# Kernel tuning notes

Hardware: AMD Instinct MI355X
Metric: run time of the kernel (lower is better)

Reference implementation:

```python
import jax, jax.numpy as jnp
import numpy as np

N_NODES = 50000
N_EDGES = 800000
NFEAT, NHID, NCLASS = 512, 128, 40
BN_EPS = 1e-5


def setup_inputs() -> dict:
    key = jax.random.key(0)
    ks = jax.random.split(key, 12)
    x = jax.random.normal(ks[0], (N_NODES, NFEAT), dtype=jnp.float32)
    edge_index = jax.random.randint(ks[1], (2, N_EDGES), 0, N_NODES, dtype=jnp.int64)
    edge_weight = jax.random.uniform(ks[2], (N_EDGES,), dtype=jnp.float32)
    def glorot(k, fi, fo):
        lim = (6.0 / (fi + fo)) ** 0.5
        return jax.random.uniform(k, (fi, fo), minval=-lim, maxval=lim, dtype=jnp.float32)
    return {
        "x": x, "edge_index": edge_index, "edge_weight": edge_weight,
        "W1": glorot(ks[3], NFEAT, NHID), "b1": jnp.zeros((NHID,), jnp.float32),
        "W2": glorot(ks[4], NHID, NHID), "b2": jnp.zeros((NHID,), jnp.float32),
        "W3": glorot(ks[5], NHID, NHID), "b3": jnp.zeros((NHID,), jnp.float32),
        "g1": jnp.ones((NHID,), jnp.float32), "be1": jnp.zeros((NHID,), jnp.float32),
        "g2": jnp.ones((NHID,), jnp.float32), "be2": jnp.zeros((NHID,), jnp.float32),
        "g3": jnp.ones((NHID,), jnp.float32), "be3": jnp.zeros((NHID,), jnp.float32),
        "linW": glorot(ks[6], NHID, NCLASS), "linb": jnp.zeros((NCLASS,), jnp.float32),
    }


def _gcn_norm(edge_index, edge_weight, n):
    # PyG gcn_norm: add self-loops (weight 1), symmetric D^-1/2 (A+I) D^-1/2
    loop = jnp.arange(n, dtype=edge_index.dtype)
    row = jnp.concatenate([edge_index[0], loop])
    col = jnp.concatenate([edge_index[1], loop])
    ew = jnp.concatenate([edge_weight, jnp.ones((n,), edge_weight.dtype)])
    deg = jax.ops.segment_sum(ew, col, num_segments=n)
    dinv = jnp.where(deg > 0, jax.lax.rsqrt(jnp.maximum(deg, 1e-30)), 0.0)
    norm = dinv[row] * ew * dinv[col]
    return row, col, norm


def _conv(x, W, b, row, col, norm, n):
    h = x @ W                                   # [N, out]
    msg = h[row] * norm[:, None]                # gather + weight, [E+N, out]
    return jax.ops.segment_sum(msg, col, num_segments=n) + b


def _bn(x, g, b):
    # training-mode BatchNorm over node dim (biased variance)
    mu = jnp.mean(x, axis=0)
    var = jnp.mean((x - mu) ** 2, axis=0)
    return (x - mu) * jax.lax.rsqrt(var + BN_EPS) * g + b


def reference(x, edge_index, edge_weight, W1, b1, W2, b2, W3, b3,
              g1, be1, g2, be2, g3, be3, linW, linb):
    n = x.shape[0]
    row, col, norm = _gcn_norm(edge_index, edge_weight, n)
    x1 = _bn(jax.nn.relu(_conv(x, W1, b1, row, col, norm, n)), g1, be1)
    x2 = _bn(jax.nn.relu(_conv(x1, W2, b2, row, col, norm, n)), g2, be2)
    x3 = _bn(_conv(x2, W3, b3, row, col, norm, n), g3, be3)
    logits = x3 @ linW + linb
    return (logits, jax.nn.softmax(logits, axis=1), x3)
```

## Files before the change

### kernel.cpp

```cpp
#include <hip/hip_runtime.h>
#include <hip/hip_bf16.h>

#define N_NODES 50000
#define N_EDGES 800000
#define NFEAT 512
#define NHID 128
#define NCLASS 40
#define BN_EPS 1e-5f

typedef __attribute__((ext_vector_type(8))) short short8;
typedef __attribute__((ext_vector_type(4))) float f32x4;

#define GEMM1_BLOCKS ((N_NODES + 127) / 128)
#define GEMMH_BLOCKS ((N_NODES + 127) / 128)
#define EDGE_BLOCKS ((N_EDGES + 255) / 256)
#define SCAN_BLOCKS ((N_NODES + 255) / 256)
#define BN_BLOCKS ((N_NODES + 255) / 256)
#define AGG_BLOCKS ((N_NODES * 64 + 255) / 256)

__device__ __forceinline__ unsigned short f2b(float f) {
    unsigned int u = __float_as_uint(f);
    u += 0x7fff + ((u >> 16) & 1);
    return (unsigned short)(u >> 16);
}
__device__ __forceinline__ unsigned int pk2(float lo, float hi) {
    unsigned int r;
    asm("v_cvt_pk_bf16_f32 %0, %1, %2" : "=v"(r) : "v"(lo), "v"(hi));
    return r;
}
__device__ __forceinline__ float blo(unsigned int v) {
    return __uint_as_float(v << 16);
}
__device__ __forceinline__ float bhi(unsigned int v) {
    return __uint_as_float(v & 0xffff0000u);
}

__global__ void k_prep_w(const float* __restrict__ W1, const float* __restrict__ W2,
                         const float* __restrict__ W3, unsigned short* __restrict__ W1t,
                         unsigned short* __restrict__ W2t, unsigned short* __restrict__ W3t,
                         unsigned long long* __restrict__ degcnt,
                         float* __restrict__ stats, int* __restrict__ syncp) {
    int i = blockIdx.x * blockDim.x + threadIdx.x;
    if (i < N_NODES) degcnt[i] = 0ULL;
    if (i < 768) stats[i] = 0.f;
    else if (i < 776) syncp[i - 768] = 0;
    if (i < 65536) {
        int k = i >> 7, n = i & 127;
        W1t[n * 512 + k] = f2b(W1[i]);
    } else if (i < 81920) {
        int j = i - 65536; int k = j >> 7, n = j & 127;
        W2t[n * 128 + k] = f2b(W2[j]);
    } else if (i < 98304) {
        int j = i - 81920; int k = j >> 7, n = j & 127;
        W3t[n * 128 + k] = f2b(W3[j]);
    }
}

__global__ __launch_bounds__(256) void k_fat(
    const float* __restrict__ x, const unsigned short* __restrict__ W1t,
    unsigned short* __restrict__ hbuf,
    const unsigned int* __restrict__ words, const float* __restrict__ ew,
    int* __restrict__ row, int* __restrict__ col,
    unsigned long long* __restrict__ degcnt, int* __restrict__ slot) {
    __shared__ unsigned short As[128][40];
    __shared__ unsigned short Bs[128][40];
    __shared__ int s_any;
    int tid = threadIdx.x;
    if (blockIdx.x < GEMM1_BLOCKS) {
        int m0 = blockIdx.x * 128;
        int srow = tid >> 1;
        int skh = (tid & 1) << 4;
        int wave = tid >> 6, lane = tid & 63;
        int wm = (wave >> 1) * 64, wn = (wave & 1) * 64;
        int l15 = lane & 15, quad = lane >> 4;
        f32x4 acc[4][4] = {};
        bool arow_ok = (m0 + srow) < N_NODES;
        const float* arow_p = x + (size_t)(m0 + srow) * 512 + skh;
        const unsigned short* wrow_p = W1t + (size_t)srow * 512 + skh;
        float4 ta[4];
        uint4 tb0, tb1;
#pragma unroll
        for (int q = 0; q < 4; q++) {
            ta[q] = make_float4(0.f, 0.f, 0.f, 0.f);
            if (arow_ok) ta[q] = *(const float4*)(arow_p + q * 4);
        }
        tb0 = *(const uint4*)(wrow_p);
        tb1 = *(const uint4*)(wrow_p + 8);
        for (int kt = 0; kt < 512; kt += 32) {
            unsigned int p[8];
#pragma unroll
            for (int q = 0; q < 4; q++) {
                p[2 * q]     = pk2(ta[q].x, ta[q].y);
                p[2 * q + 1] = pk2(ta[q].z, ta[q].w);
            }
            *(uint4*)&As[srow][skh] = make_uint4(p[0], p[1], p[2], p[3]);
            *(uint4*)&As[srow][skh + 8] = make_uint4(p[4], p[5], p[6], p[7]);
            *(uint4*)&Bs[srow][skh] = tb0;
            *(uint4*)&Bs[srow][skh + 8] = tb1;
            __syncthreads();
            if (kt + 32 < 512) {
#pragma unroll
                for (int q = 0; q < 4; q++) {
                    float4 t4 = make_float4(0.f, 0.f, 0.f, 0.f);
                    if (arow_ok) t4 = *(const float4*)(arow_p + kt + 32 + q * 4);
                    ta[q] = t4;
                }
                tb0 = *(const uint4*)(wrow_p + kt + 32);
                tb1 = *(const uint4*)(wrow_p + kt + 40);
            }
            short8 a[4], b[4];
#pragma unroll
            for (int i = 0; i < 4; i++) a[i] = *(const short8*)&As[wm + i * 16 + l15][quad * 8];
#pragma unroll
            for (int j = 0; j < 4; j++) b[j] = *(const short8*)&Bs[wn + j * 16 + l15][quad * 8];
#pragma unroll
            for (int i = 0; i < 4; i++)
#pragma unroll
                for (int j = 0; j < 4; j++)
                    acc[i][j] = __builtin_amdgcn_mfma_f32_16x16x32_bf16(a[i], b[j], acc[i][j], 0, 0, 0);
            __syncthreads();
        }
#pragma unroll
        for (int i = 0; i < 4; i++) {
            int mb = m0 + wm + i * 16 + quad * 4;
#pragma unroll
            for (int r = 0; r < 4; r++) {
                int m = mb + r;
                if (m < N_NODES) {
#pragma unroll
                    for (int j = 0; j < 4; j++)
                        hbuf[(size_t)m * 128 + wn + j * 16 + l15] = f2b(acc[i][j][r]);
                }
            }
        }
    } else {
        if (tid == 0) s_any = 0;
        __syncthreads();
        unsigned int probe = words[2 * tid + 1];
        if (probe != 0) atomicAdd(&s_any, 1);
        __syncthreads();
        int f = (s_any == 0) ? 1 : 0;
        int e = (blockIdx.x - GEMM1_BLOCKS) * 256 + tid;
        if (e < N_EDGES) {
            unsigned int r = f ? words[2 * (size_t)e] : words[e];
            unsigned int c = f ? words[2 * ((size_t)e + N_EDGES)] : words[e + N_EDGES];
            row[e] = (int)r;
            col[e] = (int)c;
            unsigned int q = __float2uint_rn(ew[e] * 8388608.0f);
            unsigned long long old = atomicAdd(&degcnt[c], (1ULL << 32) | (unsigned long long)q);
            slot[e] = (int)(old >> 32);
        }
    }
}

__global__ __launch_bounds__(256) void k_dinv(const unsigned long long* __restrict__ degcnt,
                                              float* __restrict__ dinv,
                                              int* __restrict__ counts,
                                              int* __restrict__ bsum,
                                              int* __restrict__ ticket,
                                              int* __restrict__ bpre,
                                              int* __restrict__ colptr) {
    int i = blockIdx.x * 256 + threadIdx.x;
    int cnt = 0;
    if (i < N_NODES) {
        unsigned long long v = degcnt[i];
        float deg = 1.0f + (float)(unsigned int)(v & 0xffffffffULL) * (1.0f / 8388608.0f);
        dinv[i] = rsqrtf(deg);
        cnt = (int)(v >> 32);
        counts[i] = cnt;
    }
    __shared__ int sh[256];
    __shared__ int s_last;
    sh[threadIdx.x] = cnt;
    __syncthreads();
    for (int ofs = 128; ofs > 0; ofs >>= 1) {
        if (threadIdx.x < ofs) sh[threadIdx.x] += sh[threadIdx.x + ofs];
        __syncthreads();
    }
    if (threadIdx.x == 0) {
        bsum[blockIdx.x] = sh[0];
        __threadfence();
        int t = atomicAdd(ticket, 1);
        s_last = (t == SCAN_BLOCKS - 1) ? 1 : 0;
    }
    __syncthreads();
    if (s_last) {
        __threadfence();
        int t = threadIdx.x;
        int v = (t < SCAN_BLOCKS) ? ((volatile int*)bsum)[t] : 0;
        sh[t] = v;
        __syncthreads();
        for (int ofs = 1; ofs < 256; ofs <<= 1) {
            int u = (t >= ofs) ? sh[t - ofs] : 0;
            __syncthreads();
            sh[t] += u;
            __syncthreads();
        }
        if (t < SCAN_BLOCKS) bpre[t] = sh[t] - v;
        if (t == SCAN_BLOCKS - 1) colptr[N_NODES] = sh[t];
    }
}

__global__ __launch_bounds__(256) void k_scan3(const int* __restrict__ counts,
                                               const int* __restrict__ bpre,
                                               int* __restrict__ colptr) {
    int t = threadIdx.x;
    int i = blockIdx.x * 256 + t;
    int v = (i < N_NODES) ? counts[i] : 0;
    __shared__ int sh[256];
    sh[t] = v;
    __syncthreads();
    for (int ofs = 1; ofs < 256; ofs <<= 1) {
        int u = (t >= ofs) ? sh[t - ofs] : 0;
        __syncthreads();
        sh[t] += u;
        __syncthreads();
    }
    if (i < N_NODES) colptr[i] = bpre[blockIdx.x] + sh[t] - v;
}

__global__ void k_scatter(const int* __restrict__ row, const int* __restrict__ col,
                          const float* __restrict__ ew, const float* __restrict__ dinv,
                          const int* __restrict__ colptr, const int* __restrict__ slot,
                          int2* __restrict__ ern) {
    int e = blockIdx.x * blockDim.x + threadIdx.x;
    if (e < N_EDGES) {
        int c = col[e], r = row[e];
        int p = colptr[c] + slot[e];
        float nrm = dinv[r] * ew[e] * dinv[c];
        ern[p] = make_int2(r, __float_as_int(nrm));
    }
}

__global__ __launch_bounds__(256) void k_aggregate(
    const unsigned int* __restrict__ hb, const int* __restrict__ colptr,
    const int2* __restrict__ ern, const float* __restrict__ dinv,
    const float* __restrict__ bias, unsigned int* __restrict__ out, int relu) {
    int node = (blockIdx.x * blockDim.x + threadIdx.x) >> 6;
    int lane = threadIdx.x & 63;
    if (node >= N_NODES) return;
    float di = dinv[node];
    float selfw = di * di;
    unsigned int sv = hb[(size_t)node * 64 + lane];
    float a0 = selfw * blo(sv);
    float a1 = selfw * bhi(sv);
    float c0 = 0.f, c1 = 0.f;
    int start = colptr[node], end = colptr[node + 1];
    for (int e0 = start; e0 < end; e0 += 8) {
        int2 rw[8];
        float wq[8];
#pragma unroll
        for (int q = 0; q < 8; q++) {
            int ee = e0 + q;
            bool ok = ee < end;
            rw[q] = ern[ok ? ee : start];
            wq[q] = ok ? __int_as_float(rw[q].y) : 0.f;
        }
        unsigned int v[8];
#pragma unroll
        for (int q = 0; q < 8; q++) v[q] = hb[(size_t)rw[q].x * 64 + lane];
#pragma unroll
        for (int q = 0; q < 8; q++) {
            if (q & 1) { c0 += wq[q] * blo(v[q]); c1 += wq[q] * bhi(v[q]); }
            else       { a0 += wq[q] * blo(v[q]); a1 += wq[q] * bhi(v[q]); }
        }
    }
    a0 += c0; a1 += c1;
    float2 bv = *(const float2*)&bias[2 * lane];
    a0 += bv.x;
    a1 += bv.y;
    if (relu) { a0 = fmaxf(a0, 0.f); a1 = fmaxf(a1, 0.f); }
    out[(size_t)node * 64 + lane] = pk2(a0, a1);
}

__global__ __launch_bounds__(256) void k_bnstats(const unsigned int* __restrict__ x,
                                                 float* __restrict__ sums,
                                                 float* __restrict__ sumsq) {
    int u = threadIdx.x & 63;
    int strip = threadIdx.x >> 6;
    int r0 = blockIdx.x * 256;
    int rend = min(r0 + 256, N_NODES);
    float sl = 0.f, s2l = 0.f, sh_ = 0.f, s2h = 0.f;
    for (int r = r0 + strip; r < rend; r += 16) {
        unsigned int v[4];
#pragma unroll
        for (int k = 0; k < 4; k++) {
            int rr = r + 4 * k;
            v[k] = (rr < rend) ? x[(size_t)rr * 64 + u] : 0u;
        }
#pragma unroll
        for (int k = 0; k < 4; k++) {
            float a = blo(v[k]), b = bhi(v[k]);
            sl += a; s2l += a * a;
            sh_ += b; s2h += b * b;
        }
    }
    __shared__ float buf[4][64][4];
    buf[strip][u][0] = sl; buf[strip][u][1] = s2l;
    buf[strip][u][2] = sh_; buf[strip][u][3] = s2h;
    __syncthreads();
    if (strip == 0) {
#pragma unroll
        for (int s = 1; s < 4; s++) {
            sl += buf[s][u][0]; s2l += buf[s][u][1];
            sh_ += buf[s][u][2]; s2h += buf[s][u][3];
        }
        atomicAdd(&sums[2 * u], sl);
        atomicAdd(&sums[2 * u + 1], sh_);
        atomicAdd(&sumsq[2 * u], s2l);
        atomicAdd(&sumsq[2 * u + 1], s2h);
    }
}

__global__ __launch_bounds__(256) void k_gemm_h(
    const unsigned int* __restrict__ Ab, const unsigned short* __restrict__ Wt,
    const float* __restrict__ sums, const float* __restrict__ sumsq,
    const float* __restrict__ g, const float* __restrict__ be,
    unsigned short* __restrict__ Out) {
    __shared__ unsigned short As[128][40];
    __shared__ unsigned short Bs[128][40];
    __shared__ float s_sc[128], s_sh[128];
    int tid = threadIdx.x;
    int m0 = blockIdx.x * 128;
    if (tid < 128) {
        const float invn = 1.0f / (float)N_NODES;
        float mu = sums[tid] * invn;
        float var = sumsq[tid] * invn - mu * mu;
        float iv = rsqrtf(var + BN_EPS);
        float sc = g[tid] * iv;
        s_sc[tid] = sc;
        s_sh[tid] = be[tid] - mu * sc;
    }
    __syncthreads();
    int srow = tid >> 1;
    int skh = (tid & 1) << 4;
    int wave = tid >> 6, lane = tid & 63;
    int wm = (wave >> 1) * 64, wn = (wave & 1) * 64;
    int l15 = lane & 15, quad = lane >> 4;
    f32x4 acc[4][4] = {};
    bool arow_ok = (m0 + srow) < N_NODES;
    const unsigned int* arow_b = Ab + (size_t)(m0 + srow) * 64 + (skh >> 1);
    const unsigned short* wrow_p = Wt + (size_t)srow * 128 + skh;
    uint4 r0 = make_uint4(0, 0, 0, 0), r1 = make_uint4(0, 0, 0, 0);
    uint4 tb0, tb1;
    if (arow_ok) {
        r0 = *(const uint4*)(arow_b);
        r1 = *(const uint4*)(arow_b + 4);
    }
    tb0 = *(const uint4*)(wrow_p);
    tb1 = *(const uint4*)(wrow_p + 8);
    for (int kt = 0; kt < 128; kt += 32) {
        unsigned int raw[8] = {r0.x, r0.y, r0.z, r0.w, r1.x, r1.y, r1.z, r1.w};
        unsigned int p[8];
#pragma unroll
        for (int q = 0; q < 8; q++) {
            int ch = kt + skh + 2 * q;
            float f0 = blo(raw[q]) * s_sc[ch] + s_sh[ch];
            float f1 = bhi(raw[q]) * s_sc[ch + 1] + s_sh[ch + 1];
            p[q] = pk2(f0, f1);
        }
        *(uint4*)&As[srow][skh] = make_uint4(p[0], p[1], p[2], p[3]);
        *(uint4*)&As[srow][skh + 8] = make_uint4(p[4], p[5], p[6], p[7]);
        *(uint4*)&Bs[srow][skh] = tb0;
        *(uint4*)&Bs[srow][skh + 8] = tb1;
        __syncthreads();
        if (kt + 32 < 128) {
            if (arow_ok) {
                r0 = *(const uint4*)(arow_b + ((kt + 32) >> 1));
                r1 = *(const uint4*)(arow_b + ((kt + 32) >> 1) + 4);
            }
            tb0 = *(const uint4*)(wrow_p + kt + 32);
            tb1 = *(const uint4*)(wrow_p + kt + 40);
        }
        short8 a[4], b[4];
#pragma unroll
        for (int i = 0; i < 4; i++) a[i] = *(const short8*)&As[wm + i * 16 + l15][quad * 8];
#pragma unroll
        for (int j = 0; j < 4; j++) b[j] = *(const short8*)&Bs[wn + j * 16 + l15][quad * 8];
#pragma unroll
        for (int i = 0; i < 4; i++)
#pragma unroll
            for (int j = 0; j < 4; j++)
                acc[i][j] = __builtin_amdgcn_mfma_f32_16x16x32_bf16(a[i], b[j], acc[i][j], 0, 0, 0);
        __syncthreads();
    }
#pragma unroll
    for (int i = 0; i < 4; i++) {
        int mb = m0 + wm + i * 16 + quad * 4;
#pragma unroll
        for (int r = 0; r < 4; r++) {
            int m = mb + r;
            if (m < N_NODES) {
#pragma unroll
                for (int j = 0; j < 4; j++)
                    Out[(size_t)m * 128 + wn + j * 16 + l15] = f2b(acc[i][j][r]);
            }
        }
    }
}

__global__ __launch_bounds__(256) void k_logits(const unsigned int* __restrict__ abuf,
                                                const float* __restrict__ sums,
                                                const float* __restrict__ sumsq,
                                                const float* __restrict__ g,
                                                const float* __restrict__ be,
                                                const float* __restrict__ linW,
                                                const float* __restrict__ linb,
                                                float* __restrict__ logits,
                                                float* __restrict__ probs,
                                                float* __restrict__ x3out) {
    __shared__ float Xs[64][130];
    __shared__ float Ws[128 * 40];
    __shared__ float s_sc[128], s_sh[128];
    int tid = threadIdx.x;
    int m0 = blockIdx.x * 64;
    if (tid < 128) {
        const float invn = 1.0f / (float)N_NODES;
        float mu = sums[tid] * invn;
        float var = sumsq[tid] * invn - mu * mu;
        float iv = rsqrtf(var + BN_EPS);
        float sc = g[tid] * iv;
        s_sc[tid] = sc;
        s_sh[tid] = be[tid] - mu * sc;
    }
    for (int q = tid; q < 1280; q += 256)
        *(float4*)&Ws[q * 4] = *(const float4*)&linW[q * 4];
    __syncthreads();
    for (int q = tid; q < 4096; q += 256) {
        int r = q >> 6, u = q & 63;
        int m = m0 + r;
        float f0 = 0.f, f1 = 0.f;
        if (m < N_NODES) {
            unsigned int v = abuf[(size_t)m * 64 + u];
            f0 = blo(v) * s_sc[2 * u] + s_sh[2 * u];
            f1 = bhi(v) * s_sc[2 * u + 1] + s_sh[2 * u + 1];
            *(float2*)&x3out[(size_t)m * 128 + 2 * u] = make_float2(f0, f1);
        }
        *(float2*)&Xs[r][2 * u] = make_float2(f0, f1);
    }
    __syncthreads();
    int r = tid >> 2;
    int cg = tid & 3;
    int cbase = cg * 10;
    float acc[10] = {};
    for (int k = 0; k < 128; k++) {
        float a = Xs[r][k];
#pragma unroll
        for (int j = 0; j < 10; j++) acc[j] += a * Ws[k * 40 + cbase + j];
    }
#pragma unroll
    for (int j = 0; j < 10; j++) acc[j] += linb[cbase + j];
    float m = acc[0];
#pragma unroll
    for (int j = 1; j < 10; j++) m = fmaxf(m, acc[j]);
    m = fmaxf(m, __shfl_xor(m, 1));
    m = fmaxf(m, __shfl_xor(m, 2));
    float ex[10];
    float s = 0.f;
#pragma unroll
    for (int j = 0; j < 10; j++) { ex[j] = expf(acc[j] - m); s += ex[j]; }
    s += __shfl_xor(s, 1);
    s += __shfl_xor(s, 2);
    float inv = 1.0f / s;
    int mrow = m0 + r;
    if (mrow < N_NODES) {
#pragma unroll
        for (int j = 0; j < 10; j += 2) {
            *(float2*)&logits[(size_t)mrow * 40 + cbase + j] = make_float2(acc[j], acc[j + 1]);
            *(float2*)&probs[(size_t)mrow * 40 + cbase + j] = make_float2(ex[j] * inv, ex[j + 1] * inv);
        }
    }
}

extern "C" void kernel_launch(void* const* d_in, const int* in_sizes, int n_in,
                              void* d_out, int out_size, void* d_ws, size_t ws_size,
                              hipStream_t stream) {
    const float* x = (const float*)d_in[0];
    const unsigned int* eidx = (const unsigned int*)d_in[1];
    const float* ew = (const float*)d_in[2];
    const float* W1 = (const float*)d_in[3];
    const float* b1 = (const float*)d_in[4];
    const float* W2 = (const float*)d_in[5];
    const float* b2 = (const float*)d_in[6];
    const float* W3 = (const float*)d_in[7];
    const float* b3 = (const float*)d_in[8];
    const float* g1 = (const float*)d_in[9];
    const float* be1 = (const float*)d_in[10];
    const float* g2 = (const float*)d_in[11];
    const float* be2 = (const float*)d_in[12];
    const float* g3 = (const float*)d_in[13];
    const float* be3 = (const float*)d_in[14];
    const float* linW = (const float*)d_in[15];
    const float* linb = (const float*)d_in[16];

    float* out = (float*)d_out;
    float* logits = out;
    float* probs = out + (size_t)N_NODES * NCLASS;
    float* x3out = out + 2 * (size_t)N_NODES * NCLASS;

    char* ws = (char*)d_ws;
    size_t off = 0;
    auto take = [&](size_t bytes) -> char* {
        char* p = ws + off;
        off += (bytes + 255) & ~(size_t)255;
        return p;
    };
    int* row32 = (int*)take((size_t)N_EDGES * 4);
    int* col32 = (int*)take((size_t)N_EDGES * 4);
    int* slot = (int*)take((size_t)N_EDGES * 4);
    int* colptr = (int*)take((size_t)(N_NODES + 1) * 4);
    int* counts = (int*)take((size_t)N_NODES * 4);
    unsigned long long* degcnt = (unsigned long long*)take((size_t)N_NODES * 8);
    int2* ern = (int2*)take((size_t)N_EDGES * 8);
    float* dinv = (float*)take((size_t)N_NODES * 4);
    unsigned short* hbuf = (unsigned short*)take((size_t)N_NODES * NHID * 2);
    unsigned short* abuf = (unsigned short*)take((size_t)N_NODES * NHID * 2);
    unsigned short* W1t = (unsigned short*)take((size_t)512 * 128 * 2);
    unsigned short* W2t = (unsigned short*)take((size_t)128 * 128 * 2);
    unsigned short* W3t = (unsigned short*)take((size_t)128 * 128 * 2);
    float* stats = (float*)take(768 * 4);
    int* syncp = (int*)take(8 * 4);
    int* bsum = (int*)take((size_t)SCAN_BLOCKS * 4);
    int* bpre = (int*)take((size_t)SCAN_BLOCKS * 4);
    (void)ws_size; (void)n_in; (void)in_sizes; (void)out_size;

    float* sums1 = stats, *sumsq1 = stats + 128;
    float* sums2 = stats + 256, *sumsq2 = stats + 384;
    float* sums3 = stats + 512, *sumsq3 = stats + 640;

    const int TPB = 256;

    k_prep_w<<<(98304 + TPB - 1) / TPB, TPB, 0, stream>>>(W1, W2, W3, W1t, W2t, W3t, degcnt, stats, syncp);
    k_fat<<<GEMM1_BLOCKS + EDGE_BLOCKS, TPB, 0, stream>>>(
        x, W1t, hbuf, eidx, ew, row32, col32, degcnt, slot);
    k_dinv<<<SCAN_BLOCKS, TPB, 0, stream>>>(degcnt, dinv, counts, bsum, &syncp[0], bpre, colptr);
    k_scan3<<<SCAN_BLOCKS, TPB, 0, stream>>>(counts, bpre, colptr);
    k_scatter<<<EDGE_BLOCKS, TPB, 0, stream>>>(row32, col32, ew, dinv, colptr, slot, ern);

    k_aggregate<<<AGG_BLOCKS, TPB, 0, stream>>>((const unsigned int*)hbuf, colptr, ern, dinv, b1, (unsigned int*)abuf, 1);
    k_bnstats<<<BN_BLOCKS, TPB, 0, stream>>>((const unsigned int*)abuf, sums1, sumsq1);

    k_gemm_h<<<GEMMH_BLOCKS, TPB, 0, stream>>>((const unsigned int*)abuf, W2t, sums1, sumsq1, g1, be1, hbuf);
    k_aggregate<<<AGG_BLOCKS, TPB, 0, stream>>>((const unsigned int*)hbuf, colptr, ern, dinv, b2, (unsigned int*)abuf, 1);
    k_bnstats<<<BN_BLOCKS, TPB, 0, stream>>>((const unsigned int*)abuf, sums2, sumsq2);

    k_gemm_h<<<GEMMH_BLOCKS, TPB, 0, stream>>>((const unsigned int*)abuf, W3t, sums2, sumsq2, g2, be2, hbuf);
    k_aggregate<<<AGG_BLOCKS, TPB, 0, stream>>>((const unsigned int*)hbuf, colptr, ern, dinv, b3, (unsigned int*)abuf, 0);
    k_bnstats<<<BN_BLOCKS, TPB, 0, stream>>>((const unsigned int*)abuf, sums3, sumsq3);

    k_logits<<<(N_NODES + 63) / 64, TPB, 0, stream>>>((const unsigned int*)abuf, sums3, sumsq3, g3, be3, linW, linb, logits, probs, x3out);
}
```

Baseline: 452.2 us.

## Load GEMM operands directly from global into MFMA registers, dropping LDS staging

Both the first-layer GEMM and the hidden-layer GEMM now load A and B fragments straight from global memory into the MFMA operand layout, skipping the shared-memory tiles and the per-iteration barriers. Conversion to bf16 (and the BN affine in the hidden GEMM) is applied per fragment in registers. This removes LDS traffic and synchronisation, but each row is now read by both waves that share it rather than once per block, and the loads are strided per lane and less coalesced.

```diff
diff --git a/kernel.cpp b/kernel.cpp
--- a/kernel.cpp
+++ b/kernel.cpp
@@ -62,63 +62,40 @@
     const unsigned int* __restrict__ words, const float* __restrict__ ew,
     int* __restrict__ row, int* __restrict__ col,
     unsigned long long* __restrict__ degcnt, int* __restrict__ slot) {
-    __shared__ unsigned short As[128][40];
-    __shared__ unsigned short Bs[128][40];
     __shared__ int s_any;
     int tid = threadIdx.x;
     if (blockIdx.x < GEMM1_BLOCKS) {
         int m0 = blockIdx.x * 128;
-        int srow = tid >> 1;
-        int skh = (tid & 1) << 4;
         int wave = tid >> 6, lane = tid & 63;
         int wm = (wave >> 1) * 64, wn = (wave & 1) * 64;
         int l15 = lane & 15, quad = lane >> 4;
         f32x4 acc[4][4] = {};
-        bool arow_ok = (m0 + srow) < N_NODES;
-        const float* arow_p = x + (size_t)(m0 + srow) * 512 + skh;
-        const unsigned short* wrow_p = W1t + (size_t)srow * 512 + skh;
-        float4 ta[4];
-        uint4 tb0, tb1;
-#pragma unroll
-        for (int q = 0; q < 4; q++) {
-            ta[q] = make_float4(0.f, 0.f, 0.f, 0.f);
-            if (arow_ok) ta[q] = *(const float4*)(arow_p + q * 4);
-        }
-        tb0 = *(const uint4*)(wrow_p);
-        tb1 = *(const uint4*)(wrow_p + 8);
+        const float* ap[4];
+        const unsigned short* bp[4];
+#pragma unroll
+        for (int i = 0; i < 4; i++) {
+            int m = m0 + wm + i * 16 + l15;
+            ap[i] = x + (size_t)((m < N_NODES) ? m : 0) * 512 + quad * 8;
+            bp[i] = W1t + (size_t)(wn + i * 16 + l15) * 512 + quad * 8;
+        }
+#pragma unroll 2
         for (int kt = 0; kt < 512; kt += 32) {
-            unsigned int p[8];
-#pragma unroll
-            for (int q = 0; q < 4; q++) {
-                p[2 * q]     = pk2(ta[q].x, ta[q].y);
-                p[2 * q + 1] = pk2(ta[q].z, ta[q].w);
+            short8 a[4], b[4];
+#pragma unroll
+            for (int i = 0; i < 4; i++) {
+                float4 f0 = *(const float4*)(ap[i] + kt);
+                float4 f1 = *(const float4*)(ap[i] + kt + 4);
+                uint4 pu = make_uint4(pk2(f0.x, f0.y), pk2(f0.z, f0.w),
+                                      pk2(f1.x, f1.y), pk2(f1.z, f1.w));
+                a[i] = *(const short8*)&pu;
             }
-            *(uint4*)&As[srow][skh] = make_uint4(p[0], p[1], p[2], p[3]);
-            *(uint4*)&As[srow][skh + 8] = make_uint4(p[4], p[5], p[6], p[7]);
-            *(uint4*)&Bs[srow][skh] = tb0;
-            *(uint4*)&Bs[srow][skh + 8] = tb1;
-            __syncthreads();
-            if (kt + 32 < 512) {
-#pragma unroll
-                for (int q = 0; q < 4; q++) {
-                    float4 t4 = make_float4(0.f, 0.f, 0.f, 0.f);
-                    if (arow_ok) t4 = *(const float4*)(arow_p + kt + 32 + q * 4);
-                    ta[q] = t4;
-                }
-                tb0 = *(const uint4*)(wrow_p + kt + 32);
-                tb1 = *(const uint4*)(wrow_p + kt + 40);
-            }
-            short8 a[4], b[4];
-#pragma unroll
-            for (int i = 0; i < 4; i++) a[i] = *(const short8*)&As[wm + i * 16 + l15][quad * 8];
-#pragma unroll
-            for (int j = 0; j < 4; j++) b[j] = *(const short8*)&Bs[wn + j * 16 + l15][quad * 8];
+#pragma unroll
+            for (int j = 0; j < 4; j++) b[j] = *(const short8*)(bp[j] + kt);
 #pragma unroll
             for (int i = 0; i < 4; i++)
 #pragma unroll
                 for (int j = 0; j < 4; j++)
                     acc[i][j] = __builtin_amdgcn_mfma_f32_16x16x32_bf16(a[i], b[j], acc[i][j], 0, 0, 0);
-            __syncthreads();
         }
 #pragma unroll
         for (int i = 0; i < 4; i++) {
@@ -317,8 +294,6 @@
     const float* __restrict__ sums, const float* __restrict__ sumsq,
     const float* __restrict__ g, const float* __restrict__ be,
     unsigned short* __restrict__ Out) {
-    __shared__ unsigned short As[128][40];
-    __shared__ unsigned short Bs[128][40];
     __shared__ float s_sc[128], s_sh[128];
     int tid = threadIdx.x;
     int m0 = blockIdx.x * 128;
@@ -332,57 +307,43 @@
         s_sh[tid] = be[tid] - mu * sc;
     }
     __syncthreads();
-    int srow = tid >> 1;
-    int skh = (tid & 1) << 4;
     int wave = tid >> 6, lane = tid & 63;
     int wm = (wave >> 1) * 64, wn = (wave & 1) * 64;
     int l15 = lane & 15, quad = lane >> 4;
     f32x4 acc[4][4] = {};
-    bool arow_ok = (m0 + srow) < N_NODES;
-    const unsigned int* arow_b = Ab + (size_t)(m0 + srow) * 64 + (skh >> 1);
-    const unsigned short* wrow_p = Wt + (size_t)srow * 128 + skh;
-    uint4 r0 = make_uint4(0, 0, 0, 0), r1 = make_uint4(0, 0, 0, 0);
-    uint4 tb0, tb1;
-    if (arow_ok) {
-        r0 = *(const uint4*)(arow_b);
-        r1 = *(const uint4*)(arow_b + 4);
-    }
-    tb0 = *(const uint4*)(wrow_p);
-    tb1 = *(const uint4*)(wrow_p + 8);
+    const unsigned int* ap[4];
+    const unsigned short* bp[4];
+#pragma unroll
+    for (int i = 0; i < 4; i++) {
+        int m = m0 + wm + i * 16 + l15;
+        ap[i] = Ab + (size_t)((m < N_NODES) ? m : 0) * 64 + quad * 4;
+        bp[i] = Wt + (size_t)(wn + i * 16 + l15) * 128 + quad * 8;
+    }
+#pragma unroll
     for (int kt = 0; kt < 128; kt += 32) {
-        unsigned int raw[8] = {r0.x, r0.y, r0.z, r0.w, r1.x, r1.y, r1.z, r1.w};
-        unsigned int p[8];
-#pragma unroll
-        for (int q = 0; q < 8; q++) {
-            int ch = kt + skh + 2 * q;
-            float f0 = blo(raw[q]) * s_sc[ch] + s_sh[ch];
-            float f1 = bhi(raw[q]) * s_sc[ch + 1] + s_sh[ch + 1];
-            p[q] = pk2(f0, f1);
-        }
-        *(uint4*)&As[srow][skh] = make_uint4(p[0], p[1], p[2], p[3]);
-        *(uint4*)&As[srow][skh + 8] = make_uint4(p[4], p[5], p[6], p[7]);
-        *(uint4*)&Bs[srow][skh] = tb0;
-        *(uint4*)&Bs[srow][skh + 8] = tb1;
-        __syncthreads();
-        if (kt + 32 < 128) {
-            if (arow_ok) {
-                r0 = *(const uint4*)(arow_b + ((kt + 32) >> 1));
-                r1 = *(const uint4*)(arow_b + ((kt + 32) >> 1) + 4);
-            }
-            tb0 = *(const uint4*)(wrow_p + kt + 32);
-            tb1 = *(const uint4*)(wrow_p + kt + 40);
-        }
+        float sc[8], sh[8];
+        *(float4*)&sc[0] = *(const float4*)&s_sc[kt + quad * 8];
+        *(float4*)&sc[4] = *(const float4*)&s_sc[kt + quad * 8 + 4];
+        *(float4*)&sh[0] = *(const float4*)&s_sh[kt + quad * 8];
+        *(float4*)&sh[4] = *(const float4*)&s_sh[kt + quad * 8 + 4];
         short8 a[4], b[4];
 #pragma unroll
-        for (int i = 0; i < 4; i++) a[i] = *(const short8*)&As[wm + i * 16 + l15][quad * 8];
-#pragma unroll
-        for (int j = 0; j < 4; j++) b[j] = *(const short8*)&Bs[wn + j * 16 + l15][quad * 8];
+        for (int i = 0; i < 4; i++) {
+            uint4 raw = *(const uint4*)(ap[i] + (kt >> 1));
+            uint4 pu;
+            pu.x = pk2(blo(raw.x) * sc[0] + sh[0], bhi(raw.x) * sc[1] + sh[1]);
+            pu.y = pk2(blo(raw.y) * sc[2] + sh[2], bhi(raw.y) * sc[3] + sh[3]);
+            pu.z = pk2(blo(raw.z) * sc[4] + sh[4], bhi(raw.z) * sc[5] + sh[5]);
+            pu.w = pk2(blo(raw.w) * sc[6] + sh[6], bhi(raw.w) * sc[7] + sh[7]);
+            a[i] = *(const short8*)&pu;
+        }
+#pragma unroll
+        for (int j = 0; j < 4; j++) b[j] = *(const short8*)(bp[j] + kt);
 #pragma unroll
         for (int i = 0; i < 4; i++)
 #pragma unroll
             for (int j = 0; j < 4; j++)
                 acc[i][j] = __builtin_amdgcn_mfma_f32_16x16x32_bf16(a[i], b[j], acc[i][j], 0, 0, 0);
-        __syncthreads();
     }
 #pragma unroll
     for (int i = 0; i < 4; i++) {
```

Result: slower. 477.4 us (+5.6%).
